# Kernel optimization log

Hardware: AMD Instinct MI355X
Metric: run time of the kernel (lower is better)

The kernel has to match this reference:

```python
import jax, jax.numpy as jnp
import numpy as np

# Config (mirrors CorrLayerDownsample(J=3, L=8, A=1, A_prime=1, M=256, N=256,
# num_channels=1, shift_mode='samec', mask_angles=4)). With samec + 1 channel,
# every pair is 'shifted' (mask index 1) and groups (j1,j2) are contiguous in
# the global moment order, so concatenation reproduces results_storage order.
J, L, A, M, N, NB = 3, 8, 1, 256, 256, 2
MASK_ANGLES = 4
RADII = (1, 2)  # dyadic shift radii (assumed form of create_masks_shift)

def _mask_positions():
    # shift mask 1: origin plus shifts along mask_angles directions at dyadic radii
    pos = {(0, 0)}
    for k in range(MASK_ANGLES):
        th = np.pi * k / MASK_ANGLES
        for r in RADII:
            pos.add((int(round(r * np.cos(th))), int(round(r * np.sin(th)))))
    return sorted(pos)

def _union_flat_idx(h, w):
    # row-major flat indices of the union shift mask at resolution (h, w),
    # matching torch boolean-mask indexing order (mask_downsample + mask_idx_map_1)
    return np.array(sorted(((dx % h) * w + (dy % w)) for dx, dy in _mask_positions()), dtype=np.int64)

UNION_IDX = [_union_flat_idx(M >> j, N >> j) for j in range(J)]
NSHIFT = len(UNION_IDX[0])

# per-(j1,j2) channel gather indices: la = A*L*c + A*l + a = l (A=1, c=0)
# loop order in compute_idx: l1 outer, l2 inner
LA1 = np.repeat(np.arange(L), L)
LA2 = np.tile(np.arange(L), L)

def _spectral_pad(xh, Mn, Nn):
    # zero-pad Fourier representation to (Mn, Nn) -- spectral upsampling
    m, n = xh.shape[-2], xh.shape[-1]
    if (m, n) == (Mn, Nn):
        return xh
    xs = jnp.fft.fftshift(xh, axes=(-2, -1))
    ph, pw = (Mn - m) // 2, (Nn - n) // 2
    pad = [(0, 0)] * (xh.ndim - 2) + [(ph, ph), (pw, pw)]
    xp = jnp.pad(xs, pad)
    return jnp.fft.ifftshift(xp, axes=(-2, -1)) * ((Mn * Nn) / (m * n))

def _forward(xpsi_0, xpsi_1, xpsi_2):
    xs = [xpsi_0, xpsi_1, xpsi_2]
    hats = [jnp.fft.fft2(x.astype(jnp.complex64)) for x in xs]  # [nb, C, h_j, w_j]
    la1 = jnp.asarray(LA1)
    la2 = jnp.asarray(LA2)
    outs = []
    for j1 in range(J):
        h, w = M >> j1, N >> j1
        uidx = jnp.asarray(UNION_IDX[j1])
        h1 = hats[j1][:, la1]  # [nb, P=L*L, h, w]
        for j2 in range(j1, J):
            h2 = hats[j2][:, la2]
            if j2 > j1:
                h2 = _spectral_pad(h2, h, w)  # upsample coarser scale to scale j1
            corr = jnp.fft.ifft2(h1 * jnp.conj(h2)).real  # cross-correlation map
            flat = corr.reshape(corr.shape[0], corr.shape[1], h * w)
            outs.append(flat[:, :, uidx])  # masked downsample: keep shift positions
    return jnp.concatenate(outs, axis=1)  # [nb, total_pairs, NSHIFT]

def setup_inputs():
    key = jax.random.key(0)
    ks = jax.random.split(key, 3)
    return {
        "xpsi_0": jax.random.normal(ks[0], (NB, A * L, M, N), dtype=jnp.float32),
        "xpsi_1": jax.random.normal(ks[1], (NB, A * L, M // 2, N // 2), dtype=jnp.float32),
        "xpsi_2": jax.random.normal(ks[2], (NB, A * L, M // 4, N // 4), dtype=jnp.float32),
    }

def reference(xpsi_0, xpsi_1, xpsi_2):
    return _forward(xpsi_0, xpsi_1, xpsi_2)
```

## Files before the change

### kernel.cpp

```cpp
#include <hip/hip_runtime.h>

#define PI_D 3.14159265358979323846
#define PI_F 3.14159265358979323846f


__device__ inline float rtab_val(int n, int m2, int t) {
  if (t == 0) return 1.0f;
  double th = PI_D * (double)t / (double)n;
  double v = sin(th * (double)(m2 - 1)) / sin(th) + cos(th * (double)m2);
  return (float)(v / (double)m2);
}

__global__ __launch_bounds__(256) void k_front(const float* __restrict__ X1,
                                               const float* __restrict__ X2,
                                               float* __restrict__ P1p,
                                               float* __restrict__ P2p,
                                               float* __restrict__ V01,
                                               float* __restrict__ V02,
                                               float* __restrict__ V12,
                                               float* __restrict__ out) {
  int bid = blockIdx.x;
  int t = threadIdx.x;
  if (bid == 640) {
    for (int i = t; i < 5376; i += 256) out[i] = 0.f;
    return;
  }
  if (bid < 192) {
    const float* X; float* P; int lg, nsp, idx0;
    if (bid < 128) { X = X1; P = P1p; lg = 7; nsp = 8; idx0 = bid; }
    else           { X = X2; P = P2p; lg = 6; nsp = 4; idx0 = bid - 128; }
    int ch = idx0 / nsp, split = idx0 % nsp;
    int n = 1 << lg;
    int total = n * n;
    int chunk = total / nsp;
    int b0 = split * chunk;
    const float* x = X + (size_t)ch * total + b0;
    float s = 0.f;
    for (int i = t; i < chunk; i += 256) {
      int idx = b0 + i;
      float v = x[i];
      s += (((idx >> lg) ^ idx) & 1) ? -v : v;
    }
#pragma unroll
    for (int off = 32; off > 0; off >>= 1) s += __shfl_down(s, off, 64);
    __shared__ float red[4];
    if ((t & 63) == 0) red[t >> 6] = s;
    __syncthreads();
    if (t == 0) P[ch * nsp + split] = red[0] + red[1] + red[2] + red[3];
    return;
  }
  int vbid = bid - 192;
  const float* X; float* V;
  int n1, n2, s, ch, nxg, colh, ncg;
  if (vbid < 256) {
    X = X1; V = V01; n1 = 256; n2 = 128; s = 2;
    ch = vbid >> 4; nxg = ((vbid >> 1) & 7) * 16; colh = vbid & 1; ncg = 2;
  } else if (vbid < 384) {
    int w = vbid - 256;
    X = X2; V = V02; n1 = 256; n2 = 64; s = 4;
    ch = w >> 3; nxg = ((w >> 1) & 3) * 16; colh = w & 1; ncg = 2;
  } else {
    int w = vbid - 384;
    X = X2; V = V12; n1 = 128; n2 = 64; s = 2;
    ch = w >> 2; nxg = (w & 3) * 16; colh = 0; ncg = 2;
  }
  __shared__ float Rl[256];
  __shared__ float Xs[16 * 128];
  for (int i = t; i < n1; i += 256) Rl[i] = rtab_val(n1, n2, i);
  const float4* xch4 =
      (const float4*)(X + (size_t)ch * n2 * n2 + (size_t)nxg * n2);
  int nx4 = (16 * n2) >> 2;
  for (int i = t; i < nx4; i += 256) ((float4*)Xs)[i] = xch4[i];
  __syncthreads();
  int myq = (t & 63) + colh * 128;
  int nxq = t >> 6;
  int mask = n1 - 1;
  float acc[4][2];
#pragma unroll
  for (int r = 0; r < 4; ++r)
#pragma unroll
    for (int c = 0; c < 2; ++c) acc[r][c] = 0.f;
  for (int ny = 0; ny < n2; ++ny) {
    float xv[4];
#pragma unroll
    for (int r = 0; r < 4; ++r) xv[r] = Xs[(4 * nxq + r) * n2 + ny];
#pragma unroll
    for (int c = 0; c < 2; ++c) {
      float rv = Rl[(myq + 64 * c - s * ny) & mask];
#pragma unroll
      for (int r = 0; r < 4; ++r) acc[r][c] += xv[r] * rv;
    }
  }
  float* vch = V + (size_t)ch * n2 * n1;
#pragma unroll
  for (int r = 0; r < 4; ++r)
    for (int c = 0; c < 2; ++c)
      vch[(size_t)(nxg + 4 * nxq + r) * n1 + myq + 64 * c] = acc[r][c];
}

__global__ __launch_bounds__(256) void k_main(const float* __restrict__ X0,
                                              const float* __restrict__ X1,
                                              const float* __restrict__ X2,
                                              const float* __restrict__ V01,
                                              const float* __restrict__ V02,
                                              const float* __restrict__ V12,
                                              const float* __restrict__ P1p,
                                              const float* __restrict__ P2p,
                                              float* __restrict__ out) {
  __shared__ float smem[8448];
  float* sRl = smem;
  float* sh = smem + 256;
  int u = blockIdx.x;
  int t = threadIdx.x;
  int lane = t & 63;
  int wv = t >> 6;

  float accC[8][7];
#pragma unroll
  for (int i = 0; i < 8; ++i)
#pragma unroll
    for (int p = 0; p < 7; ++p) accC[i][p] = 0.f;

  int base, b, l2;

  if (u < 640) {
    const float* V; const float* Pp; const float* A1b;
    int n1, n2, s, ch, chunk, nsp, lgn1; float inv;
    if (u < 256)      { V = V01; Pp = P1p; nsp = 8; A1b = X0; n1 = 256; n2 = 128; s = 2; inv = 1.f / (128.f * 128.f); ch = u >> 4; chunk = u & 15; lgn1 = 8; base = 64; }
    else if (u < 512) { int w = u - 256; V = V02; Pp = P2p; nsp = 4; A1b = X0; n1 = 256; n2 = 64; s = 4; inv = 1.f / (64.f * 64.f); ch = w >> 4; chunk = w & 15; lgn1 = 8; base = 128; }
    else              { int w = u - 512; V = V12; Pp = P2p; nsp = 4; A1b = X1; n1 = 128; n2 = 64; s = 2; inv = 1.f / (64.f * 64.f); ch = w >> 3; chunk = w & 7; lgn1 = 7; base = 256; }
    int mask = n1 - 1;
    for (int i = t; i < n1; i += 256) sRl[i] = rtab_val(n1, n2, i);
    int mxg = chunk * 16;
    b = ch >> 3; l2 = ch & 7;
    const float* vch = V + (size_t)ch * n2 * n1;
    float Pv = 0.f;
    for (int i = 0; i < nsp; ++i) Pv += Pp[ch * nsp + i];
    float a = PI_F / (float)s;
    int per = 2 * s;
    if (n1 == 256) {
      int cid = t & 63;
      float4 acc[5];
#pragma unroll
      for (int j = 0; j < 5; ++j) acc[j] = make_float4(0.f, 0.f, 0.f, 0.f);
      for (int nx0 = 0; nx0 < n2; nx0 += 32) {
        __syncthreads();
        const float4* s4 = (const float4*)(vch + (size_t)nx0 * 256);
        for (int i = t; i < 2048; i += 256) ((float4*)sh)[i] = s4[i];
        __syncthreads();
#pragma unroll 8
        for (int k = 0; k < 32; ++k) {
          int nx = nx0 + k;
          float4 vv = *(const float4*)&sh[k * 256 + 4 * cid];
#pragma unroll
          for (int j = 0; j < 5; ++j) {
            int mx = (mxg - 2 + wv + 4 * j) & mask;
            float rv = sRl[(mx - s * nx) & mask];
            acc[j].x += rv * vv.x; acc[j].y += rv * vv.y;
            acc[j].z += rv * vv.z; acc[j].w += rv * vv.w;
          }
        }
      }
      __syncthreads();
      float smy[4];
#pragma unroll
      for (int j = 0; j < 4; ++j) smy[j] = sinf(a * (float)((4 * cid + j) & (per - 1)));
#pragma unroll
      for (int j = 0; j < 5; ++j) {
        int rl = wv + 4 * j;
        if (rl < 19) {
          int mx = (mxg - 2 + rl) & mask;
          float q = inv * sinf(a * (float)(mx & (per - 1))) * Pv;
          float4 o = acc[j];
          o.x -= q * smy[0]; o.y -= q * smy[1]; o.z -= q * smy[2]; o.w -= q * smy[3];
          *(float4*)&sh[rl * 256 + 4 * cid] = o;
        }
      }
    } else {
      int cid = t & 31;
      int owner = t >> 5;
      float4 acc[3];
#pragma unroll
      for (int j = 0; j < 3; ++j) acc[j] = make_float4(0.f, 0.f, 0.f, 0.f);
      __syncthreads();
      {
        const float4* s4 = (const float4*)vch;
        for (int i = t; i < 2048; i += 256) ((float4*)sh)[i] = s4[i];
      }
      __syncthreads();
#pragma unroll 8
      for (int nx = 0; nx < 64; ++nx) {
        float4 vv = *(const float4*)&sh[nx * 128 + 4 * cid];
#pragma unroll
        for (int j = 0; j < 3; ++j) {
          int mx = (mxg - 2 + owner + 8 * j) & 127;
          float rv = sRl[(mx - 2 * nx) & 127];
          acc[j].x += rv * vv.x; acc[j].y += rv * vv.y;
          acc[j].z += rv * vv.z; acc[j].w += rv * vv.w;
        }
      }
      __syncthreads();
      float smy[4];
#pragma unroll
      for (int j = 0; j < 4; ++j) smy[j] = sinf(a * (float)((4 * cid + j) & 3));
#pragma unroll
      for (int j = 0; j < 3; ++j) {
        int rl = owner + 8 * j;
        if (rl < 19) {
          int mx = (mxg - 2 + rl) & 127;
          float q = inv * sinf(a * (float)(mx & 3)) * Pv;
          float4 o = acc[j];
          o.x -= q * smy[0]; o.y -= q * smy[1]; o.z -= q * smy[2]; o.w -= q * smy[3];
          *(float4*)&sh[rl * 128 + 4 * cid] = o;
        }
      }
    }
    __syncthreads();
    int lgtpr = lgn1 - 2;
    int tpr = 1 << lgtpr;
    int rif = 256 >> lgtpr;
    int rid = t >> lgtpr;
    int cid2 = t & (tpr - 1);
    int ty = cid2 * 4;
    int tym = (ty - 4) & mask;
    int n1sq = n1 * n1;
    const float* A1 = A1b + (size_t)(b * 8) * n1sq;
    for (int rr = 0; rr < 16; rr += rif) {
      int ri = rr + rid;
      const float* r0 = &sh[(ri + 2) * n1];
      const float* r1 = &sh[(ri + 1) * n1];
      const float* r2 = &sh[ri * n1];
      const float* r3 = &sh[(ri + 3) * n1];
      float4 a0 = *(const float4*)(r0 + tym);
      float4 b0 = *(const float4*)(r0 + ty);
      float4 a1 = *(const float4*)(r1 + tym);
      float4 b1 = *(const float4*)(r1 + ty);
      float4 b2 = *(const float4*)(r2 + ty);
      float4 a3 = *(const float4*)(r3 + tym);
      float4 b3 = *(const float4*)(r3 + ty);
      const float* rA = A1 + (size_t)(mxg + ri) * n1 + ty;
#pragma unroll
      for (int l1 = 0; l1 < 8; ++l1) {
        float4 xv = *(const float4*)(rA + (size_t)l1 * n1sq);
        accC[l1][0] += xv.x * b0.x + xv.y * b0.y + xv.z * b0.z + xv.w * b0.w;
        accC[l1][1] += xv.x * a0.w + xv.y * b0.x + xv.z * b0.y + xv.w * b0.z;
        accC[l1][2] += xv.x * a0.z + xv.y * a0.w + xv.z * b0.x + xv.w * b0.y;
        accC[l1][3] += xv.x * b1.x + xv.y * b1.y + xv.z * b1.z + xv.w * b1.w;
        accC[l1][4] += xv.x * a1.w + xv.y * b1.x + xv.z * b1.y + xv.w * b1.z;
        accC[l1][5] += xv.x * b2.x + xv.y * b2.y + xv.z * b2.z + xv.w * b2.w;
        accC[l1][6] += xv.x * a3.w + xv.y * b3.x + xv.z * b3.y + xv.w * b3.z;
      }
    }
  } else {
    int w = u - 640;
    const float* Ab; int loc, lgn1, lgc;
    if (w < 256)      { loc = w;       Ab = X0; lgn1 = 8; lgc = 4; base = 0;   }
    else if (w < 384) { loc = w - 256; Ab = X1; lgn1 = 7; lgc = 3; base = 192; }
    else              { loc = w - 384; Ab = X2; lgn1 = 6; lgc = 2; base = 320; }
    int n1 = 1 << lgn1;
    int mask = n1 - 1;
    int n1sq = n1 * n1;
    int chunk = loc & ((1 << lgc) - 1);
    int bl2 = loc >> lgc;
    b = bl2 >> 3; l2 = bl2 & 7;
    const float* A1 = Ab + (size_t)(b * 8) * n1sq;
    const float* A2 = Ab + (size_t)(b * 8 + l2) * n1sq;
    int lgtpr = lgn1 - 2;
    int tpr = 1 << lgtpr;
    int rif = 256 >> lgtpr;
    int rid = t >> lgtpr;
    int cid2 = t & (tpr - 1);
    int ty = cid2 * 4;
    int tym = (ty - 4) & mask;
    for (int rr = 0; rr < 16; rr += rif) {
      int row = chunk * 16 + rr + rid;
      const float* r0 = A2 + (size_t)row * n1;
      const float* r1 = A2 + (size_t)((row - 1) & mask) * n1;
      const float* r2 = A2 + (size_t)((row - 2) & mask) * n1;
      const float* r3 = A2 + (size_t)((row + 1) & mask) * n1;
      float4 a0 = *(const float4*)(r0 + tym);
      float4 b0 = *(const float4*)(r0 + ty);
      float4 a1 = *(const float4*)(r1 + tym);
      float4 b1 = *(const float4*)(r1 + ty);
      float4 b2 = *(const float4*)(r2 + ty);
      float4 a3 = *(const float4*)(r3 + tym);
      float4 b3 = *(const float4*)(r3 + ty);
      const float* rA = A1 + (size_t)row * n1 + ty;
#pragma unroll
      for (int l1 = 0; l1 < 8; ++l1) {
        float4 xv = *(const float4*)(rA + (size_t)l1 * n1sq);
        accC[l1][0] += xv.x * b0.x + xv.y * b0.y + xv.z * b0.z + xv.w * b0.w;
        accC[l1][1] += xv.x * a0.w + xv.y * b0.x + xv.z * b0.y + xv.w * b0.z;
        accC[l1][2] += xv.x * a0.z + xv.y * a0.w + xv.z * b0.x + xv.w * b0.y;
        accC[l1][3] += xv.x * b1.x + xv.y * b1.y + xv.z * b1.z + xv.w * b1.w;
        accC[l1][4] += xv.x * a1.w + xv.y * b1.x + xv.z * b1.y + xv.w * b1.z;
        accC[l1][5] += xv.x * b2.x + xv.y * b2.y + xv.z * b2.z + xv.w * b2.w;
        accC[l1][6] += xv.x * a3.w + xv.y * b3.x + xv.z * b3.y + xv.w * b3.z;
      }
    }
  }
  float* af = &accC[0][0];
#pragma unroll
  for (int j = 0; j < 56; ++j) {
    float v = af[j];
    v += __shfl_down(v, 32, 64);
    v += __shfl_down(v, 16, 64);
    af[j] = v;
  }
  __syncthreads();
  if (lane < 16) {
    float* rowp = sh + (wv * 16 + lane) * 60;
#pragma unroll
    for (int j = 0; j < 14; ++j)
      *(float4*)&rowp[4 * j] =
          make_float4(af[4 * j], af[4 * j + 1], af[4 * j + 2], af[4 * j + 3]);
  }
  __syncthreads();
  if (t < 224) {
    int v = t >> 2, q = t & 3;
    float s2 = 0.f;
#pragma unroll
    for (int i = 0; i < 16; ++i) s2 += sh[(q * 16 + i) * 60 + v];
    s2 += __shfl_down(s2, 2, 64);
    s2 += __shfl_down(s2, 1, 64);
    if (q == 0) {
      int l1o = v / 7, p = v % 7;
      atomicAdd(&out[((size_t)b * 384 + base + l1o * 8 + l2) * 7 + p], s2);
    }
  }
}

extern "C" void kernel_launch(void* const* d_in, const int* in_sizes, int n_in,
                              void* d_out, int out_size, void* d_ws, size_t ws_size,
                              hipStream_t stream) {
  const float* X0 = (const float*)d_in[0];
  const float* X1 = (const float*)d_in[1];
  const float* X2 = (const float*)d_in[2];
  float* out = (float*)d_out;
  float* ws = (float*)d_ws;

  float* V01 = ws + 2359296;
  float* V02 = ws + 2883584;
  float* V12 = ws + 3145728;
  float* P1p = ws + 3276800;
  float* P2p = ws + 3276928;

  k_front<<<641, 256, 0, stream>>>(X1, X2, P1p, P2p, V01, V02, V12, out);
  k_main<<<1088, 256, 0, stream>>>(X0, X1, X2, V01, V02, V12, P1p, P2p, out);
}
```

Baseline: 106.9 us.

## Stream V directly from global with prefetch and use contiguous row ownership

The first-stage k_main loops no longer stage V tiles through shared memory. Each thread reads its float4 of V straight from global memory with a one-step register prefetch. Rows are reassigned so each wave or thread group owns contiguous output rows, which lets a precomputed shifted-window table R4 supply four or five R coefficients in one shared load. This removes the per-tile __syncthreads barriers and the shared-memory staging traffic, and shrinks shared memory (which may help occupancy). In exchange it relies on cache hits for the global V reads, since each V row is now read separately by every wave in the block.

```diff
diff --git a/kernel.cpp b/kernel.cpp
--- a/kernel.cpp
+++ b/kernel.cpp
@@ -51,18 +51,18 @@
   }
   int vbid = bid - 192;
   const float* X; float* V;
-  int n1, n2, s, ch, nxg, colh, ncg;
+  int n1, n2, s, ch, nxg, colh;
   if (vbid < 256) {
     X = X1; V = V01; n1 = 256; n2 = 128; s = 2;
-    ch = vbid >> 4; nxg = ((vbid >> 1) & 7) * 16; colh = vbid & 1; ncg = 2;
+    ch = vbid >> 4; nxg = ((vbid >> 1) & 7) * 16; colh = vbid & 1;
   } else if (vbid < 384) {
     int w = vbid - 256;
     X = X2; V = V02; n1 = 256; n2 = 64; s = 4;
-    ch = w >> 3; nxg = ((w >> 1) & 3) * 16; colh = w & 1; ncg = 2;
+    ch = w >> 3; nxg = ((w >> 1) & 3) * 16; colh = w & 1;
   } else {
     int w = vbid - 384;
     X = X2; V = V12; n1 = 128; n2 = 64; s = 2;
-    ch = w >> 2; nxg = (w & 3) * 16; colh = 0; ncg = 2;
+    ch = w >> 2; nxg = (w & 3) * 16; colh = 0;
   }
   __shared__ float Rl[256];
   __shared__ float Xs[16 * 128];
@@ -107,9 +107,9 @@
                                               const float* __restrict__ P1p,
                                               const float* __restrict__ P2p,
                                               float* __restrict__ out) {
-  __shared__ float smem[8448];
-  float* sRl = smem;
-  float* sh = smem + 256;
+  __shared__ float sRl[256];
+  __shared__ float4 R4[256];
+  __shared__ float sh[4864];
   int u = blockIdx.x;
   int t = threadIdx.x;
   int lane = t & 63;
@@ -131,6 +131,11 @@
     else              { int w = u - 512; V = V12; Pp = P2p; nsp = 4; A1b = X1; n1 = 128; n2 = 64; s = 2; inv = 1.f / (64.f * 64.f); ch = w >> 3; chunk = w & 7; lgn1 = 7; base = 256; }
     int mask = n1 - 1;
     for (int i = t; i < n1; i += 256) sRl[i] = rtab_val(n1, n2, i);
+    __syncthreads();
+    for (int i = t; i < n1; i += 256)
+      R4[i] = make_float4(sRl[i], sRl[(i + 1) & mask], sRl[(i + 2) & mask],
+                          sRl[(i + 3) & mask]);
+    __syncthreads();
     int mxg = chunk * 16;
     b = ch >> 3; l2 = ch & 7;
     const float* vch = V + (size_t)ch * n2 * n1;
@@ -140,34 +145,31 @@
     int per = 2 * s;
     if (n1 == 256) {
       int cid = t & 63;
+      int rb = mxg - 2 + 5 * wv;
       float4 acc[5];
 #pragma unroll
       for (int j = 0; j < 5; ++j) acc[j] = make_float4(0.f, 0.f, 0.f, 0.f);
-      for (int nx0 = 0; nx0 < n2; nx0 += 32) {
-        __syncthreads();
-        const float4* s4 = (const float4*)(vch + (size_t)nx0 * 256);
-        for (int i = t; i < 2048; i += 256) ((float4*)sh)[i] = s4[i];
-        __syncthreads();
-#pragma unroll 8
-        for (int k = 0; k < 32; ++k) {
-          int nx = nx0 + k;
-          float4 vv = *(const float4*)&sh[k * 256 + 4 * cid];
-#pragma unroll
-          for (int j = 0; j < 5; ++j) {
-            int mx = (mxg - 2 + wv + 4 * j) & mask;
-            float rv = sRl[(mx - s * nx) & mask];
-            acc[j].x += rv * vv.x; acc[j].y += rv * vv.y;
-            acc[j].z += rv * vv.z; acc[j].w += rv * vv.w;
-          }
+      float4 vv = *(const float4*)(vch + 4 * cid);
+      for (int nx = 0; nx < n2; ++nx) {
+        float4 vvn;
+        if (nx + 1 < n2) vvn = *(const float4*)(vch + (size_t)(nx + 1) * 256 + 4 * cid);
+        int ib = (rb - s * nx) & mask;
+        float4 r03 = R4[ib];
+        float r4v = sRl[(ib + 4) & mask];
+        float rv[5] = {r03.x, r03.y, r03.z, r03.w, r4v};
+#pragma unroll
+        for (int j = 0; j < 5; ++j) {
+          acc[j].x += rv[j] * vv.x; acc[j].y += rv[j] * vv.y;
+          acc[j].z += rv[j] * vv.z; acc[j].w += rv[j] * vv.w;
         }
-      }
-      __syncthreads();
+        vv = vvn;
+      }
       float smy[4];
 #pragma unroll
       for (int j = 0; j < 4; ++j) smy[j] = sinf(a * (float)((4 * cid + j) & (per - 1)));
 #pragma unroll
       for (int j = 0; j < 5; ++j) {
-        int rl = wv + 4 * j;
+        int rl = 5 * wv + j;
         if (rl < 19) {
           int mx = (mxg - 2 + rl) & mask;
           float q = inv * sinf(a * (float)(mx & (per - 1))) * Pv;
@@ -179,33 +181,30 @@
     } else {
       int cid = t & 31;
       int owner = t >> 5;
+      int rb = mxg - 2 + 3 * owner;
       float4 acc[3];
 #pragma unroll
       for (int j = 0; j < 3; ++j) acc[j] = make_float4(0.f, 0.f, 0.f, 0.f);
-      __syncthreads();
-      {
-        const float4* s4 = (const float4*)vch;
-        for (int i = t; i < 2048; i += 256) ((float4*)sh)[i] = s4[i];
-      }
-      __syncthreads();
-#pragma unroll 8
+      float4 vv = *(const float4*)(vch + 4 * cid);
       for (int nx = 0; nx < 64; ++nx) {
-        float4 vv = *(const float4*)&sh[nx * 128 + 4 * cid];
+        float4 vvn;
+        if (nx + 1 < 64) vvn = *(const float4*)(vch + (size_t)(nx + 1) * 128 + 4 * cid);
+        int ib = (rb - 2 * nx) & 127;
+        float4 r03 = R4[ib];
+        float rv[3] = {r03.x, r03.y, r03.z};
 #pragma unroll
         for (int j = 0; j < 3; ++j) {
-          int mx = (mxg - 2 + owner + 8 * j) & 127;
-          float rv = sRl[(mx - 2 * nx) & 127];
-          acc[j].x += rv * vv.x; acc[j].y += rv * vv.y;
-          acc[j].z += rv * vv.z; acc[j].w += rv * vv.w;
+          acc[j].x += rv[j] * vv.x; acc[j].y += rv[j] * vv.y;
+          acc[j].z += rv[j] * vv.z; acc[j].w += rv[j] * vv.w;
         }
-      }
-      __syncthreads();
+        vv = vvn;
+      }
       float smy[4];
 #pragma unroll
       for (int j = 0; j < 4; ++j) smy[j] = sinf(a * (float)((4 * cid + j) & 3));
 #pragma unroll
       for (int j = 0; j < 3; ++j) {
-        int rl = owner + 8 * j;
+        int rl = 3 * owner + j;
         if (rl < 19) {
           int mx = (mxg - 2 + rl) & 127;
           float q = inv * sinf(a * (float)(mx & 3)) * Pv;
```

After: 103.6 us (median of 2 runs). 1.03x faster.
